# Kernel tuning notes

Measured on AMD Instinct MI355X. Metric: run time of the kernel, lower is better.

## Reference

```python
import jax, jax.numpy as jnp
import numpy as np

DIN = 1024
DOUT = 1024
NUM_HEAD = 16
HEAD_DIM = DIN // NUM_HEAD  # 64
SEQ = 2048
BS = 4


def setup_inputs() -> dict:
    key = jax.random.key(0)
    ks = jax.random.split(key, 9)
    s_in = 1.0 / np.sqrt(DIN)
    s_out = 1.0 / np.sqrt(DOUT)
    return {
        "x": jax.random.normal(ks[0], (BS, SEQ, DIN), dtype=jnp.float32),
        "Wq": jax.random.normal(ks[1], (DIN, DOUT), dtype=jnp.float32) * s_in,
        "bq": jax.random.normal(ks[2], (DOUT,), dtype=jnp.float32) * s_in,
        "Wk": jax.random.normal(ks[3], (DIN, DOUT), dtype=jnp.float32) * s_in,
        "bk": jax.random.normal(ks[4], (DOUT,), dtype=jnp.float32) * s_in,
        "Wv": jax.random.normal(ks[5], (DIN, DOUT), dtype=jnp.float32) * s_in,
        "bv": jax.random.normal(ks[6], (DOUT,), dtype=jnp.float32) * s_in,
        "Wo": jax.random.normal(ks[7], (DOUT, DOUT), dtype=jnp.float32) * s_out,
        "bo": jax.random.normal(ks[8], (DOUT,), dtype=jnp.float32) * s_out,
    }


def reference(x, Wq, bq, Wk, bk, Wv, bv, Wo, bo):
    bs, n, _ = x.shape
    # projections -> [bs, n, H, hd] -> [bs, H, n, hd]
    def split_heads(t):
        return t.reshape(bs, n, NUM_HEAD, HEAD_DIM).transpose(0, 2, 1, 3)

    q = split_heads(x @ Wq + bq)
    k = split_heads(x @ Wk + bk)
    v = split_heads(x @ Wv + bv)

    # full [bs, H, n, n] scores, causal mask, scaled softmax
    scores = jnp.einsum("bhqd,bhkd->bhqk", q, k)
    causal = jnp.tril(jnp.ones((n, n), dtype=bool))
    scores = jnp.where(causal, scores, -jnp.inf)
    att = jax.nn.softmax(scores / np.sqrt(HEAD_DIM), axis=-1)

    ctx = jnp.einsum("bhqk,bhkd->bhqd", att, v)
    ctx = ctx.transpose(0, 2, 1, 3).reshape(bs, n, DOUT)
    return ctx @ Wo + bo
```

## Files before the change

kernel.cpp:

```cpp
#include <hip/hip_runtime.h>
#include <hip/hip_bf16.h>
#include <stdint.h>

#define DIN   1024
#define DOUT  1024
#define NHEAD 16
#define HDIM  64
#define SEQL  2048
#define BSZ   4
#define MTOT  (BSZ*SEQL)
#define KDIM  1024

typedef __bf16 bf16x8 __attribute__((ext_vector_type(8)));
typedef float  f32x4  __attribute__((ext_vector_type(4)));

__device__ __forceinline__ f32x4 mfma16(bf16x8 a, bf16x8 b, f32x4 c) {
    return __builtin_amdgcn_mfma_f32_16x16x32_bf16(a, b, c, 0, 0, 0);
}

__device__ __forceinline__ void gl_lds16(const void* gsrc, void* ldst) {
    __builtin_amdgcn_global_load_lds(
        (const __attribute__((address_space(1))) uint32_t*)gsrc,
        (__attribute__((address_space(3))) uint32_t*)ldst, 16, 0, 0);
}

__device__ __forceinline__ unsigned short f2bf(float f) {
    union { __hip_bfloat16 h; unsigned short u; } cv;
    cv.h = __float2bfloat16(f);
    return cv.u;
}

__global__ void cvt_bf16(const float4* __restrict__ in, ushort4* __restrict__ out, int n4) {
    int idx = blockIdx.x * blockDim.x + threadIdx.x;
    int stride = gridDim.x * blockDim.x;
    for (int i = idx; i < n4; i += stride) {
        float4 v = in[i];
        ushort4 o;
        o.x = f2bf(v.x); o.y = f2bf(v.y); o.z = f2bf(v.z); o.w = f2bf(v.w);
        out[i] = o;
    }
}

__global__ void transpose_cvt3(const float* __restrict__ W0, const float* __restrict__ W1,
                               const float* __restrict__ W2, __hip_bfloat16* __restrict__ Wt3) {
    __shared__ __hip_bfloat16 t[32][33];
    const int tx = threadIdx.x, ty = threadIdx.y;
    const int bx = blockIdx.x, by = blockIdx.y, z = blockIdx.z;
    const float* W = (z == 0) ? W0 : (z == 1) ? W1 : W2;
    __hip_bfloat16* Wt = Wt3 + (size_t)z * DOUT * DIN;
#pragma unroll
    for (int r = 0; r < 4; ++r)
        t[ty + 8*r][tx] = __float2bfloat16(W[(size_t)(by*32 + ty + 8*r) * DOUT + bx*32 + tx]);
    __syncthreads();
#pragma unroll
    for (int r = 0; r < 4; ++r)
        Wt[(size_t)(bx*32 + ty + 8*r) * DIN + by*32 + tx] = t[tx][ty + 8*r];
}

__global__ void transpose_cvt(const float* __restrict__ W, __hip_bfloat16* __restrict__ Wt) {
    __shared__ __hip_bfloat16 t[32][33];
    const int tx = threadIdx.x, ty = threadIdx.y;
    const int bx = blockIdx.x, by = blockIdx.y;
#pragma unroll
    for (int r = 0; r < 4; ++r)
        t[ty + 8*r][tx] = __float2bfloat16(W[(size_t)(by*32 + ty + 8*r) * DOUT + bx*32 + tx]);
    __syncthreads();
#pragma unroll
    for (int r = 0; r < 4; ++r)
        Wt[(size_t)(bx*32 + ty + 8*r) * DIN + by*32 + tx] = t[tx][ty + 8*r];
}

template <int EPI>
__global__ __launch_bounds__(256)
void gemm_mfma(const __hip_bfloat16* __restrict__ A,
               const __hip_bfloat16* __restrict__ Bt,
               const float* __restrict__ b0, const float* __restrict__ b1,
               void* __restrict__ o0, void* __restrict__ o1,
               float scale)
{
    __shared__ alignas(16) __hip_bfloat16 As[2][4][128][8];
    __shared__ alignas(16) __hip_bfloat16 Bs[2][4][128][8];

    const int tid  = threadIdx.x;
    const int w    = tid >> 6;
    const int lane = tid & 63;
    const int g    = lane >> 4;
    const int r    = lane & 15;
    const int wr   = w >> 1, wc = w & 1;

    const int row0 = blockIdx.y * 128;
    const int col0 = blockIdx.x * 128;

    f32x4 acc[4][4];
#pragma unroll
    for (int m = 0; m < 4; ++m)
#pragma unroll
        for (int n = 0; n < 4; ++n) acc[m][n] = (f32x4)0.0f;

    auto stage = [&](int buf, int kt) {
        const __hip_bfloat16* ga = A  + (size_t)(row0 + lane) * KDIM + kt*32 + 8*w;
        const __hip_bfloat16* gb = Bt + (size_t)(col0 + lane) * KDIM + kt*32 + 8*w;
        gl_lds16(ga,            &As[buf][w][0][0]);
        gl_lds16(ga + 64*KDIM,  &As[buf][w][64][0]);
        gl_lds16(gb,            &Bs[buf][w][0][0]);
        gl_lds16(gb + 64*KDIM,  &Bs[buf][w][64][0]);
    };

    stage(0, 0);
    __syncthreads();

    const int NKT = KDIM / 32;
    for (int kt = 0; kt < NKT; ++kt) {
        const int cur = kt & 1;
        if (kt + 1 < NKT) stage(cur ^ 1, kt + 1);

        bf16x8 af[4], bfr[4];
#pragma unroll
        for (int m = 0; m < 4; ++m)
            af[m] = *reinterpret_cast<const bf16x8*>(&As[cur][g][64*wr + 16*m + r][0]);
#pragma unroll
        for (int n = 0; n < 4; ++n)
            bfr[n] = *reinterpret_cast<const bf16x8*>(&Bs[cur][g][64*wc + 16*n + r][0]);

#pragma unroll
        for (int m = 0; m < 4; ++m)
#pragma unroll
            for (int n = 0; n < 4; ++n) {
                if (EPI == 1) acc[m][n] = mfma16(af[m], bfr[n], acc[m][n]);
                else          acc[m][n] = mfma16(bfr[n], af[m], acc[m][n]);
            }

        __syncthreads();
    }

    if (EPI == 0) {
        const int slab = col0 >> 10;
        const float* bp = (slab == 0) ? b0 : b1;
        __hip_bfloat16* op = (__hip_bfloat16*)((slab == 0) ? o0 : o1);
        const float sc = (slab == 0) ? scale : 1.0f;
#pragma unroll
        for (int m = 0; m < 4; ++m) {
            const int rowg = row0 + 64*wr + 16*m + r;
            const int bb = rowg >> 11, sq = rowg & (SEQL-1);
#pragma unroll
            for (int n = 0; n < 4; ++n) {
                const int c2 = (col0 & 1023) + 64*wc + 16*n + 4*g;
                const int hh = c2 >> 6, dd = c2 & (HDIM-1);
                const float4 bv4 = *reinterpret_cast<const float4*>(&bp[c2]);
                ushort4 ov;
                ov.x = f2bf((acc[m][n][0] + bv4.x) * sc);
                ov.y = f2bf((acc[m][n][1] + bv4.y) * sc);
                ov.z = f2bf((acc[m][n][2] + bv4.z) * sc);
                ov.w = f2bf((acc[m][n][3] + bv4.w) * sc);
                *reinterpret_cast<ushort4*>(
                    &op[(((size_t)(bb*NHEAD + hh) * SEQL + sq) << 6) + dd]) = ov;
            }
        }
    } else if (EPI == 1) {
#pragma unroll
        for (int n = 0; n < 4; ++n) {
            const int colg = col0 + 64*wc + 16*n + r;
            const int hh = colg >> 6, dd = colg & (HDIM-1);
            const float bv_ = b0[colg];
#pragma unroll
            for (int m = 0; m < 4; ++m) {
                const int rowg0 = row0 + 64*wr + 16*m + 4*g;
                const int bb = rowg0 >> 11, sq0 = rowg0 & (SEQL-1);
                ushort4 ov;
                ov.x = f2bf(acc[m][n][0] + bv_);
                ov.y = f2bf(acc[m][n][1] + bv_);
                ov.z = f2bf(acc[m][n][2] + bv_);
                ov.w = f2bf(acc[m][n][3] + bv_);
                *reinterpret_cast<ushort4*>(
                    &((__hip_bfloat16*)o0)[((size_t)(bb*NHEAD + hh) * HDIM + dd) * SEQL + sq0]) = ov;
            }
        }
    } else {
#pragma unroll
        for (int m = 0; m < 4; ++m) {
            const int rowg = row0 + 64*wr + 16*m + r;
#pragma unroll
            for (int n = 0; n < 4; ++n) {
                const int colg0 = col0 + 64*wc + 16*n + 4*g;
                const float4 bv4 = *reinterpret_cast<const float4*>(&b0[colg0]);
                float4 ov;
                ov.x = acc[m][n][0] + bv4.x;
                ov.y = acc[m][n][1] + bv4.y;
                ov.z = acc[m][n][2] + bv4.z;
                ov.w = acc[m][n][3] + bv4.w;
                *reinterpret_cast<float4*>(&((float*)o0)[(size_t)rowg * DOUT + colg0]) = ov;
            }
        }
    }
}

__global__ __launch_bounds__(256)
void attn_fwd(const __hip_bfloat16* __restrict__ Q,
              const __hip_bfloat16* __restrict__ K,
              const __hip_bfloat16* __restrict__ Vt,
              __hip_bfloat16* __restrict__ ctx)
{
    __shared__ alignas(16) __hip_bfloat16 Ps[4][2][16][64];
    __shared__ alignas(16) f32x4 Om[2][64][8];
    __shared__ float Ml[2][64][5];

    const int tid  = threadIdx.x;
    const int w    = tid >> 6;
    const int lane = tid & 63;
    const int g    = lane >> 4;
    const int r    = lane & 15;
    const int swz  = (r & 7) << 3;
    const int pp   = w >> 1;
    const int half = w & 1;

    const int bh = blockIdx.x;
    const int b  = bh >> 4, h = bh & 15;

    const __hip_bfloat16* Qh = Q  + (size_t)bh * SEQL * HDIM;
    const __hip_bfloat16* Kh = K  + (size_t)bh * SEQL * HDIM;
    const __hip_bfloat16* Vh = Vt + (size_t)bh * HDIM * SEQL;

    const int sp = blockIdx.y * 2 + pp;

#pragma unroll 1
    for (int ti = 0; ti < 2; ++ti) {
        const int strip = ti ? (63 - sp) : sp;
        const int qb = strip * 32;

        bf16x8 qf[2][2];
#pragma unroll
        for (int m = 0; m < 2; ++m)
#pragma unroll
            for (int hh = 0; hh < 2; ++hh)
                qf[m][hh] = *reinterpret_cast<const bf16x8*>(
                    Qh + (size_t)(qb + 16*m + r) * HDIM + 32*hh + 8*g);

        f32x4 o[2][4];
        float mrow[2], lrow[2];
#pragma unroll
        for (int m = 0; m < 2; ++m) {
#pragma unroll
            for (int n = 0; n < 4; ++n) o[m][n] = (f32x4)0.0f;
            mrow[m] = -1e30f; lrow[m] = 0.0f;
        }

        const int nst = ((qb + 31) >> 6) + 1;
        const int ns2 = (nst + 1) >> 1;
        const int k0  = half ? ns2 : 0;
        const int k1  = half ? nst : ns2;

#pragma unroll 1
        for (int kt = k0; kt < k1; ++kt) {
            const int key0 = kt * 64;

            bf16x8 kf[4][2];
#pragma unroll
            for (int c = 0; c < 4; ++c)
#pragma unroll
                for (int hh = 0; hh < 2; ++hh)
                    kf[c][hh] = *reinterpret_cast<const bf16x8*>(
                        Kh + (size_t)(key0 + 16*c + r) * HDIM + 32*hh + 8*g);

            f32x4 s[2][4];
            __builtin_amdgcn_s_setprio(1);
#pragma unroll
            for (int m = 0; m < 2; ++m)
#pragma unroll
                for (int c = 0; c < 4; ++c) {
                    f32x4 t = (f32x4)0.0f;
                    t = mfma16(kf[c][0], qf[m][0], t);
                    t = mfma16(kf[c][1], qf[m][1], t);
                    s[m][c] = t;
                }
            __builtin_amdgcn_s_setprio(0);

            if (kt == nst - 1) {
#pragma unroll
                for (int m = 0; m < 2; ++m) {
                    const int qrow = qb + 16*m + r;
#pragma unroll
                    for (int c = 0; c < 4; ++c) {
                        const int kb = key0 + 16*c + 4*g;
#pragma unroll
                        for (int j = 0; j < 4; ++j)
                            if (kb + j > qrow) s[m][c][j] = -1e30f;
                    }
                }
            }

#pragma unroll
            for (int m = 0; m < 2; ++m) {
                float t0 = fmaxf(fmaxf(s[m][0][0], s[m][0][1]), fmaxf(s[m][0][2], s[m][0][3]));
                float t1 = fmaxf(fmaxf(s[m][1][0], s[m][1][1]), fmaxf(s[m][1][2], s[m][1][3]));
                float t2 = fmaxf(fmaxf(s[m][2][0], s[m][2][1]), fmaxf(s[m][2][2], s[m][2][3]));
                float t3 = fmaxf(fmaxf(s[m][3][0], s[m][3][1]), fmaxf(s[m][3][2], s[m][3][3]));
                float pm = fmaxf(fmaxf(t0, t1), fmaxf(t2, t3));
                pm = fmaxf(pm, __shfl_xor(pm, 16));
                pm = fmaxf(pm, __shfl_xor(pm, 32));

                if (__any(pm > mrow[m] + 11.0f)) {
                    const float mnew = fmaxf(mrow[m], pm);
                    const float fac  = exp2f(mrow[m] - mnew);
                    mrow[m] = mnew;
                    lrow[m] *= fac;
#pragma unroll
                    for (int n = 0; n < 4; ++n) o[m][n] *= fac;
                }

                float p[4][4];
#pragma unroll
                for (int c = 0; c < 4; ++c)
#pragma unroll
                    for (int j = 0; j < 4; ++j)
                        p[c][j] = exp2f(s[m][c][j] - mrow[m]);

                float u0 = (p[0][0] + p[0][1]) + (p[0][2] + p[0][3]);
                float u1 = (p[1][0] + p[1][1]) + (p[1][2] + p[1][3]);
                float u2 = (p[2][0] + p[2][1]) + (p[2][2] + p[2][3]);
                float u3 = (p[3][0] + p[3][1]) + (p[3][2] + p[3][3]);
                float ps = (u0 + u1) + (u2 + u3);
                ps += __shfl_xor(ps, 16);
                ps += __shfl_xor(ps, 32);
                lrow[m] += ps;

#pragma unroll
                for (int c = 0; c < 4; ++c) {
                    ushort4 pk4;
                    pk4.x = f2bf(p[c][0]); pk4.y = f2bf(p[c][1]);
                    pk4.z = f2bf(p[c][2]); pk4.w = f2bf(p[c][3]);
                    *reinterpret_cast<ushort4*>(&Ps[w][m][r][(16*c + 4*g) ^ swz]) = pk4;
                }
            }

            bf16x8 pf[2][2];
#pragma unroll
            for (int m = 0; m < 2; ++m)
#pragma unroll
                for (int hh = 0; hh < 2; ++hh)
                    pf[m][hh] = *reinterpret_cast<const bf16x8*>(
                        &Ps[w][m][r][(32*hh + 8*g) ^ swz]);

            __builtin_amdgcn_s_setprio(1);
#pragma unroll
            for (int n = 0; n < 4; ++n) {
                bf16x8 vf0 = *reinterpret_cast<const bf16x8*>(
                    Vh + (size_t)(16*n + r) * SEQL + key0 + 8*g);
                bf16x8 vf1 = *reinterpret_cast<const bf16x8*>(
                    Vh + (size_t)(16*n + r) * SEQL + key0 + 32 + 8*g);
#pragma unroll
                for (int m = 0; m < 2; ++m) {
                    o[m][n] = mfma16(vf0, pf[m][0], o[m][n]);
                    o[m][n] = mfma16(vf1, pf[m][1], o[m][n]);
                }
            }
            __builtin_amdgcn_s_setprio(0);
        }

        if (half) {
#pragma unroll
            for (int m = 0; m < 2; ++m)
#pragma unroll
                for (int n = 0; n < 4; ++n)
                    Om[pp][lane][(m*4 + n) ^ (lane & 7)] = o[m][n];
            Ml[pp][lane][0] = mrow[0];
            Ml[pp][lane][1] = mrow[1];
            Ml[pp][lane][2] = lrow[0];
            Ml[pp][lane][3] = lrow[1];
        }
        __syncthreads();
        if (!half) {
#pragma unroll
            for (int m = 0; m < 2; ++m) {
                const float m1 = Ml[pp][lane][m];
                const float l1 = Ml[pp][lane][2 + m];
                const float M  = fmaxf(mrow[m], m1);
                const float f0 = exp2f(mrow[m] - M);
                const float f1 = exp2f(m1 - M);
                const float L  = lrow[m] * f0 + l1 * f1;
                const float inv = 1.0f / L;
                const size_t rowbase = (size_t)(b*SEQL + qb + 16*m + r) * DOUT + h*HDIM;
#pragma unroll
                for (int n = 0; n < 4; ++n) {
                    const f32x4 o1 = Om[pp][lane][(m*4 + n) ^ (lane & 7)];
                    ushort4 ov;
                    ov.x = f2bf((o[m][n][0]*f0 + o1[0]*f1) * inv);
                    ov.y = f2bf((o[m][n][1]*f0 + o1[1]*f1) * inv);
                    ov.z = f2bf((o[m][n][2]*f0 + o1[2]*f1) * inv);
                    ov.w = f2bf((o[m][n][3]*f0 + o1[3]*f1) * inv);
                    *reinterpret_cast<ushort4*>(&ctx[rowbase + 16*n + 4*g]) = ov;
                }
            }
        }
        __syncthreads();
    }
}

extern "C" void kernel_launch(void* const* d_in, const int* in_sizes, int n_in,
                              void* d_out, int out_size, void* d_ws, size_t ws_size,
                              hipStream_t stream) {
    const float* x  = (const float*)d_in[0];
    const float* Wq = (const float*)d_in[1];
    const float* bq = (const float*)d_in[2];
    const float* Wk = (const float*)d_in[3];
    const float* bk = (const float*)d_in[4];
    const float* Wv = (const float*)d_in[5];
    const float* bv = (const float*)d_in[6];
    const float* Wo = (const float*)d_in[7];
    const float* bo = (const float*)d_in[8];
    float* out = (float*)d_out;
    (void)in_sizes; (void)n_in; (void)out_size; (void)ws_size;

    char* ws = (char*)d_ws;
    __hip_bfloat16* xb  = (__hip_bfloat16*)ws;
    __hip_bfloat16* Wt3 = (__hip_bfloat16*)(ws + (16u << 20));
    __hip_bfloat16* Wot = (__hip_bfloat16*)(ws + (22u << 20));
    __hip_bfloat16* Qb  = (__hip_bfloat16*)(ws + (24u << 20));
    __hip_bfloat16* Kb  = Qb + (size_t)MTOT * DOUT;
    __hip_bfloat16* Vtb = Kb + (size_t)MTOT * DOUT;
    __hip_bfloat16* ctx = xb;

    cvt_bf16<<<2048, 256, 0, stream>>>((const float4*)x, (ushort4*)xb, MTOT * DIN / 4);

    dim3 tb(32, 8);
    transpose_cvt3<<<dim3(32, 32, 3), tb, 0, stream>>>(Wq, Wk, Wv, Wt3);
    transpose_cvt <<<dim3(32, 32),    tb, 0, stream>>>(Wo, Wot);

    dim3 gqk(2*DOUT / 128, MTOT / 128);
    gemm_mfma<0><<<gqk, 256, 0, stream>>>(xb, Wt3, bq, bk, Qb, Kb,
                                          0.125f * 1.44269504088896f);
    dim3 gv(DOUT / 128, MTOT / 128);
    gemm_mfma<1><<<gv, 256, 0, stream>>>(xb, Wt3 + (size_t)2*DOUT*DIN, bv, nullptr,
                                         Vtb, nullptr, 1.0f);

    dim3 ag(BSZ * NHEAD, 16);
    attn_fwd<<<ag, 256, 0, stream>>>(Qb, Kb, Vtb, ctx);

    gemm_mfma<2><<<gv, 256, 0, stream>>>(ctx, Wot, bo, nullptr,
                                         out, nullptr, 1.0f);
}
```

Before: 308.4 us.

## Pack bf16 conversions, prefetch V with K, defer row-sum and max reductions

Replaces per-element bf16 conversion with a bit-trick round-to-nearest that packs two values via v_perm, used in every conversion epilogue. In the attention loop, V fragments are now loaded together with K at the top of each iteration through incrementing pointers, so their latency overlaps the QK and softmax work. The cross-lane max shuffle runs only inside the rare rescale branch, and the row-sum shuffle moves out of the loop to a single reduction at the end. The risks are higher register pressure from holding both K and V fragments, and the manual rounding not handling NaN the way the library conversion does.

Result: no change. 313.4 us (+1.6%).

```diff
diff --git a/kernel.cpp b/kernel.cpp
--- a/kernel.cpp
+++ b/kernel.cpp
@@ -30,13 +30,22 @@
     return cv.u;
 }
 
-__global__ void cvt_bf16(const float4* __restrict__ in, ushort4* __restrict__ out, int n4) {
+__device__ __forceinline__ unsigned int pk_bf16(float lo, float hi) {
+    unsigned int a = __float_as_uint(lo);
+    unsigned int b = __float_as_uint(hi);
+    a += 0x7FFFu + ((a >> 16) & 1u);
+    b += 0x7FFFu + ((b >> 16) & 1u);
+    return __builtin_amdgcn_perm(b, a, 0x07060302u);
+}
+
+__global__ void cvt_bf16(const float4* __restrict__ in, uint2* __restrict__ out, int n4) {
     int idx = blockIdx.x * blockDim.x + threadIdx.x;
     int stride = gridDim.x * blockDim.x;
     for (int i = idx; i < n4; i += stride) {
         float4 v = in[i];
-        ushort4 o;
-        o.x = f2bf(v.x); o.y = f2bf(v.y); o.z = f2bf(v.z); o.w = f2bf(v.w);
+        uint2 o;
+        o.x = pk_bf16(v.x, v.y);
+        o.y = pk_bf16(v.z, v.w);
         out[i] = o;
     }
 }
@@ -147,12 +156,10 @@
                 const int c2 = (col0 & 1023) + 64*wc + 16*n + 4*g;
                 const int hh = c2 >> 6, dd = c2 & (HDIM-1);
                 const float4 bv4 = *reinterpret_cast<const float4*>(&bp[c2]);
-                ushort4 ov;
-                ov.x = f2bf((acc[m][n][0] + bv4.x) * sc);
-                ov.y = f2bf((acc[m][n][1] + bv4.y) * sc);
-                ov.z = f2bf((acc[m][n][2] + bv4.z) * sc);
-                ov.w = f2bf((acc[m][n][3] + bv4.w) * sc);
-                *reinterpret_cast<ushort4*>(
+                uint2 ov;
+                ov.x = pk_bf16((acc[m][n][0] + bv4.x) * sc, (acc[m][n][1] + bv4.y) * sc);
+                ov.y = pk_bf16((acc[m][n][2] + bv4.z) * sc, (acc[m][n][3] + bv4.w) * sc);
+                *reinterpret_cast<uint2*>(
                     &op[(((size_t)(bb*NHEAD + hh) * SEQL + sq) << 6) + dd]) = ov;
             }
         }
@@ -166,12 +173,10 @@
             for (int m = 0; m < 4; ++m) {
                 const int rowg0 = row0 + 64*wr + 16*m + 4*g;
                 const int bb = rowg0 >> 11, sq0 = rowg0 & (SEQL-1);
-                ushort4 ov;
-                ov.x = f2bf(acc[m][n][0] + bv_);
-                ov.y = f2bf(acc[m][n][1] + bv_);
-                ov.z = f2bf(acc[m][n][2] + bv_);
-                ov.w = f2bf(acc[m][n][3] + bv_);
-                *reinterpret_cast<ushort4*>(
+                uint2 ov;
+                ov.x = pk_bf16(acc[m][n][0] + bv_, acc[m][n][1] + bv_);
+                ov.y = pk_bf16(acc[m][n][2] + bv_, acc[m][n][3] + bv_);
+                *reinterpret_cast<uint2*>(
                     &((__hip_bfloat16*)o0)[((size_t)(bb*NHEAD + hh) * HDIM + dd) * SEQL + sq0]) = ov;
             }
         }
@@ -249,17 +254,31 @@
         const int k0  = half ? ns2 : 0;
         const int k1  = half ? nst : ns2;
 
+        const __hip_bfloat16* kp01 = Kh + (size_t)(k0*64 + r) * HDIM + 8*g;
+        const __hip_bfloat16* kp23 = kp01 + 32*HDIM;
+        const __hip_bfloat16* vp0  = Vh + (size_t)r * SEQL + (size_t)k0*64 + 8*g;
+        const __hip_bfloat16* vp1  = vp0 + (size_t)16*SEQL;
+        const __hip_bfloat16* vp2  = vp0 + (size_t)32*SEQL;
+        const __hip_bfloat16* vp3  = vp0 + (size_t)48*SEQL;
+
 #pragma unroll 1
         for (int kt = k0; kt < k1; ++kt) {
             const int key0 = kt * 64;
 
-            bf16x8 kf[4][2];
-#pragma unroll
-            for (int c = 0; c < 4; ++c)
-#pragma unroll
-                for (int hh = 0; hh < 2; ++hh)
-                    kf[c][hh] = *reinterpret_cast<const bf16x8*>(
-                        Kh + (size_t)(key0 + 16*c + r) * HDIM + 32*hh + 8*g);
+            bf16x8 kf[4][2], vf[4][2];
+#pragma unroll
+            for (int hh = 0; hh < 2; ++hh) {
+                kf[0][hh] = *reinterpret_cast<const bf16x8*>(kp01 + hh*32);
+                kf[1][hh] = *reinterpret_cast<const bf16x8*>(kp01 + 16*HDIM + hh*32);
+                kf[2][hh] = *reinterpret_cast<const bf16x8*>(kp23 + hh*32);
+                kf[3][hh] = *reinterpret_cast<const bf16x8*>(kp23 + 16*HDIM + hh*32);
+                vf[0][hh] = *reinterpret_cast<const bf16x8*>(vp0 + hh*32);
+                vf[1][hh] = *reinterpret_cast<const bf16x8*>(vp1 + hh*32);
+                vf[2][hh] = *reinterpret_cast<const bf16x8*>(vp2 + hh*32);
+                vf[3][hh] = *reinterpret_cast<const bf16x8*>(vp3 + hh*32);
+            }
+            kp01 += 64*HDIM; kp23 += 64*HDIM;
+            vp0 += 64; vp1 += 64; vp2 += 64; vp3 += 64;
 
             f32x4 s[2][4];
             __builtin_amdgcn_s_setprio(1);
@@ -294,11 +313,11 @@
                 float t1 = fmaxf(fmaxf(s[m][1][0], s[m][1][1]), fmaxf(s[m][1][2], s[m][1][3]));
                 float t2 = fmaxf(fmaxf(s[m][2][0], s[m][2][1]), fmaxf(s[m][2][2], s[m][2][3]));
                 float t3 = fmaxf(fmaxf(s[m][3][0], s[m][3][1]), fmaxf(s[m][3][2], s[m][3][3]));
-                float pm = fmaxf(fmaxf(t0, t1), fmaxf(t2, t3));
-                pm = fmaxf(pm, __shfl_xor(pm, 16));
-                pm = fmaxf(pm, __shfl_xor(pm, 32));
-
-                if (__any(pm > mrow[m] + 11.0f)) {
+                float pml = fmaxf(fmaxf(t0, t1), fmaxf(t2, t3));
+
+                if (__any(pml > mrow[m] + 11.0f)) {
+                    float pm = fmaxf(pml, __shfl_xor(pml, 16));
+                    pm = fmaxf(pm, __shfl_xor(pm, 32));
                     const float mnew = fmaxf(mrow[m], pm);
                     const float fac  = exp2f(mrow[m] - mnew);
                     mrow[m] = mnew;
@@ -318,17 +337,14 @@
                 float u1 = (p[1][0] + p[1][1]) + (p[1][2] + p[1][3]);
                 float u2 = (p[2][0] + p[2][1]) + (p[2][2] + p[2][3]);
                 float u3 = (p[3][0] + p[3][1]) + (p[3][2] + p[3][3]);
-                float ps = (u0 + u1) + (u2 + u3);
-                ps += __shfl_xor(ps, 16);
-                ps += __shfl_xor(ps, 32);
-                lrow[m] += ps;
+                lrow[m] += (u0 + u1) + (u2 + u3);
 
 #pragma unroll
                 for (int c = 0; c < 4; ++c) {
-                    ushort4 pk4;
-                    pk4.x = f2bf(p[c][0]); pk4.y = f2bf(p[c][1]);
-                    pk4.z = f2bf(p[c][2]); pk4.w = f2bf(p[c][3]);
-                    *reinterpret_cast<ushort4*>(&Ps[w][m][r][(16*c + 4*g) ^ swz]) = pk4;
+                    uint2 pk;
+                    pk.x = pk_bf16(p[c][0], p[c][1]);
+                    pk.y = pk_bf16(p[c][2], p[c][3]);
+                    *reinterpret_cast<uint2*>(&Ps[w][m][r][(16*c + 4*g) ^ swz]) = pk;
                 }
             }
 
@@ -342,18 +358,19 @@
 
             __builtin_amdgcn_s_setprio(1);
 #pragma unroll
-            for (int n = 0; n < 4; ++n) {
-                bf16x8 vf0 = *reinterpret_cast<const bf16x8*>(
-                    Vh + (size_t)(16*n + r) * SEQL + key0 + 8*g);
-                bf16x8 vf1 = *reinterpret_cast<const bf16x8*>(
-                    Vh + (size_t)(16*n + r) * SEQL + key0 + 32 + 8*g);
+            for (int n = 0; n < 4; ++n)
 #pragma unroll
                 for (int m = 0; m < 2; ++m) {
-                    o[m][n] = mfma16(vf0, pf[m][0], o[m][n]);
-                    o[m][n] = mfma16(vf1, pf[m][1], o[m][n]);
-                }
-            }
+                    o[m][n] = mfma16(vf[n][0], pf[m][0], o[m][n]);
+                    o[m][n] = mfma16(vf[n][1], pf[m][1], o[m][n]);
+                }
             __builtin_amdgcn_s_setprio(0);
+        }
+
+#pragma unroll
+        for (int m = 0; m < 2; ++m) {
+            lrow[m] += __shfl_xor(lrow[m], 16);
+            lrow[m] += __shfl_xor(lrow[m], 32);
         }
 
         if (half) {
@@ -382,12 +399,12 @@
 #pragma unroll
                 for (int n = 0; n < 4; ++n) {
                     const f32x4 o1 = Om[pp][lane][(m*4 + n) ^ (lane & 7)];
-                    ushort4 ov;
-                    ov.x = f2bf((o[m][n][0]*f0 + o1[0]*f1) * inv);
-                    ov.y = f2bf((o[m][n][1]*f0 + o1[1]*f1) * inv);
-                    ov.z = f2bf((o[m][n][2]*f0 + o1[2]*f1) * inv);
-                    ov.w = f2bf((o[m][n][3]*f0 + o1[3]*f1) * inv);
-                    *reinterpret_cast<ushort4*>(&ctx[rowbase + 16*n + 4*g]) = ov;
+                    uint2 ov;
+                    ov.x = pk_bf16((o[m][n][0]*f0 + o1[0]*f1) * inv,
+                                   (o[m][n][1]*f0 + o1[1]*f1) * inv);
+                    ov.y = pk_bf16((o[m][n][2]*f0 + o1[2]*f1) * inv,
+                                   (o[m][n][3]*f0 + o1[3]*f1) * inv);
+                    *reinterpret_cast<uint2*>(&ctx[rowbase + 16*n + 4*g]) = ov;
                 }
             }
         }
@@ -419,7 +436,7 @@
     __hip_bfloat16* Vtb = Kb + (size_t)MTOT * DOUT;
     __hip_bfloat16* ctx = xb;
 
-    cvt_bf16<<<2048, 256, 0, stream>>>((const float4*)x, (ushort4*)xb, MTOT * DIN / 4);
+    cvt_bf16<<<2048, 256, 0, stream>>>((const float4*)x, (uint2*)xb, MTOT * DIN / 4);
 
     dim3 tb(32, 8);
     transpose_cvt3<<<dim3(32, 32, 3), tb, 0, stream>>>(Wq, Wk, Wv, Wt3);
```
